# Optimization experiments

Hardware: AMD Instinct MI355X
Metric: run time of the kernel (lower is better)

The kernel has to match this reference:

```python
import jax, jax.numpy as jnp
import numpy as np

N = 20000      # nodes
E = 320000     # edges
IN = 300       # input_channel
HID = 100      # hidden_channel (= heads*out_channels with heads=1)
R = 50         # num_relations
B = 8          # num_bases (the 4th positional arg 'heads'=8 lands on num_bases in PyG RGATConv)
HEADS = 1
CLS = 3
Q = 64         # number of query (aspect) nodes
EPS = 1e-16


def setup_inputs() -> dict:
    key = jax.random.key(0)
    ks = jax.random.split(key, 16)
    x = jax.random.normal(ks[0], (N, IN), jnp.float32)
    edge_index = jax.random.randint(ks[1], (2, E), 0, N)
    edge_type = jax.random.randint(ks[2], (E,), 0, R)
    query_indices = jax.random.randint(ks[3], (Q,), 0, N)

    def w(k, shape, scale):
        return jax.random.normal(k, shape, jnp.float32) * scale

    comp1 = w(ks[4], (R, B), 0.3)
    basis1 = w(ks[5], (B, IN, HEADS * HID), 1.0 / np.sqrt(IN))
    q1 = w(ks[6], (HEADS * HID, HEADS), 0.1)
    k1 = w(ks[7], (HEADS * HID, HEADS), 0.1)
    b1 = jnp.zeros((HEADS * HID,), jnp.float32)
    comp2 = w(ks[8], (R, B), 0.3)
    basis2 = w(ks[9], (B, HID, HEADS * HID), 1.0 / np.sqrt(HID))
    q2 = w(ks[10], (HEADS * HID, HEADS), 0.1)
    k2 = w(ks[11], (HEADS * HID, HEADS), 0.1)
    b2 = jnp.zeros((HEADS * HID,), jnp.float32)
    Wl = w(ks[12], (CLS, HID), 1.0 / np.sqrt(HID))
    bl = jnp.zeros((CLS,), jnp.float32)
    return dict(x=x, edge_index=edge_index, edge_type=edge_type,
                query_indices=query_indices,
                comp1=comp1, basis1=basis1, q1=q1, k1=k1, b1=b1,
                comp2=comp2, basis2=basis2, q2=q2, k2=k2, b2=b2,
                Wl=Wl, bl=bl)


def segment_softmax(alpha, seg, num_segments):
    # numerically-stable softmax over edges grouped by destination node
    m = jax.ops.segment_max(alpha, seg, num_segments=num_segments)  # [N, H]
    e = jnp.exp(alpha - m[seg])
    s = jax.ops.segment_sum(e, seg, num_segments=num_segments)
    return e / (s[seg] + EPS)


def rgat_conv(x, edge_index, edge_type, comp, basis, q, k, b):
    # basis-decomposed per-relation weight: [R, in, H*out]
    W = jnp.einsum('rb,bio->rio', comp, basis)
    # transform every node under every relation once, then gather per edge
    xt = jnp.einsum('ni,rio->nro', x, W)          # [N, R, H*out]
    src, dst = edge_index[0], edge_index[1]        # j -> i (source_to_target)
    xi = xt[dst, edge_type]                        # [E, H*out]
    xj = xt[src, edge_type]                        # [E, H*out]
    qi = xi @ q                                    # [E, H]
    kj = xj @ k                                    # [E, H]
    alpha = jax.nn.leaky_relu(qi + kj, 0.2)        # additive self-attention
    alpha = segment_softmax(alpha, dst, N)         # across-relation softmax
    msg = xj.reshape(E, HEADS, HID) * alpha[:, :, None]
    out = jax.ops.segment_sum(msg, dst, num_segments=N)  # [N, H, out]
    return out.reshape(N, HEADS * HID) + b         # concat=True


def reference(x, edge_index, edge_type, query_indices,
              comp1, basis1, q1, k1, b1,
              comp2, basis2, q2, k2, b2, Wl, bl):
    h = jax.nn.relu(rgat_conv(x, edge_index, edge_type, comp1, basis1, q1, k1, b1))
    h = jax.nn.relu(rgat_conv(h, edge_index, edge_type, comp2, basis2, q2, k2, b2))
    pooled = h[query_indices].mean(axis=0)          # [HID]
    return pooled @ Wl.T + bl                       # [CLS]
```

## Files before the change

### kernel.cpp

```cpp
#include <hip/hip_runtime.h>
#include <math.h>

#define N_NODES 20000
#define E_EDGES 320000
#define IN_CH   300
#define HID     100
#define R_REL   50
#define NB      8
#define CLS     3
#define NQ      64
#define OUTW    800
#define ZW      128
#define SCAN_BLKS ((N_NODES + 255) / 256)

typedef unsigned short ushort_t;
typedef __attribute__((ext_vector_type(8))) short     short8;
typedef __attribute__((ext_vector_type(8))) unsigned short ushort8;
typedef __attribute__((ext_vector_type(4))) float     f32x4;
typedef __attribute__((ext_vector_type(2))) float     f32x2;

__device__ __forceinline__ ushort_t f2bf_rne(float f) {
    unsigned u = __float_as_uint(f);
    unsigned r = (u + 0x7fffu + ((u >> 16) & 1u)) >> 16;
    return (ushort_t)r;
}
__device__ __forceinline__ float bf2f(ushort_t u) {
    return __uint_as_float((unsigned)u << 16);
}

__global__ __launch_bounds__(256) void zero_deg2(int* __restrict__ dd,
                                                 int* __restrict__ ds) {
    int i = blockIdx.x * 256 + threadIdx.x;
    if (i < N_NODES) { dd[i] = 0; ds[i] = 0; }
}

__global__ __launch_bounds__(256) void hist2_kernel(
        const int* __restrict__ ei, int* __restrict__ dd,
        int* __restrict__ ds) {
    int e = blockIdx.x * 256 + threadIdx.x;
    if (e < E_EDGES) {
        atomicAdd(&dd[ei[E_EDGES + e]], 1);
        atomicAdd(&ds[ei[e]], 1);
    }
}

__global__ __launch_bounds__(256) void scan1_kernel(
        const int* __restrict__ deg, int* __restrict__ rowptr,
        int* __restrict__ bsum) {
    __shared__ int s[256];
    int tid = threadIdx.x;
    int idx = blockIdx.x * 256 + tid;
    int v = (idx < N_NODES) ? deg[idx] : 0;
    s[tid] = v; __syncthreads();
    #pragma unroll
    for (int off = 1; off < 256; off <<= 1) {
        int t = (tid >= off) ? s[tid - off] : 0;
        __syncthreads();
        s[tid] += t;
        __syncthreads();
    }
    if (idx < N_NODES) rowptr[idx] = s[tid] - v;
    if (tid == 255) bsum[blockIdx.x] = s[255];
}

__global__ __launch_bounds__(128) void scan2_kernel(int* __restrict__ bsum,
                                                    int* __restrict__ rowptr) {
    __shared__ int s[128];
    int tid = threadIdx.x;
    int v = (tid < SCAN_BLKS) ? bsum[tid] : 0;
    s[tid] = v; __syncthreads();
    #pragma unroll
    for (int off = 1; off < 128; off <<= 1) {
        int t = (tid >= off) ? s[tid - off] : 0;
        __syncthreads();
        s[tid] += t;
        __syncthreads();
    }
    if (tid < SCAN_BLKS) bsum[tid] = s[tid] - v;
    if (tid == 0) rowptr[N_NODES] = E_EDGES;
}

__global__ __launch_bounds__(256) void scan3_kernel(
        int* __restrict__ rowptr, const int* __restrict__ bsum,
        int* __restrict__ cursor) {
    int idx = blockIdx.x * 256 + threadIdx.x;
    if (idx < N_NODES) {
        int v = rowptr[idx] + bsum[blockIdx.x];
        rowptr[idx] = v;
        cursor[idx] = v;
    }
}

__global__ __launch_bounds__(256) void scatter_both(
        const int* __restrict__ ei, const int* __restrict__ et,
        int* __restrict__ cur_d, int* __restrict__ cur_s,
        int* __restrict__ skey, int* __restrict__ skey_s) {
    int e = blockIdx.x * 256 + threadIdx.x;
    if (e >= E_EDGES) return;
    int s = ei[e], d = ei[E_EDGES + e], rt = et[e];
    int p = atomicAdd(&cur_d[d], 1);
    skey[p] = (s << 6) | rt;
    int qp = atomicAdd(&cur_s[s], 1);
    skey_s[qp] = (p << 6) | rt;
}

__global__ __launch_bounds__(256) void split_bt_kernel(
        const float* __restrict__ basis, ushort_t* __restrict__ Bt,
        int K, int Kp) {
    int idx = blockIdx.x * 256 + threadIdx.x;
    if (idx >= OUTW * Kp) return;
    int n = idx / Kp, k = idx - n * Kp;
    int b = n / HID, o = n - b * HID;
    float v = 0.f;
    if (k < K) v = basis[((size_t)b * K + k) * HID + o];
    Bt[idx] = f2bf_rne(v);
}

#define BM 128
#define BN 160
__global__ __launch_bounds__(256) void gemm_mfma(
        const float* __restrict__ A, const ushort_t* __restrict__ Bt,
        float* __restrict__ C, int M, int K, int Kp, int do_relu) {
    __shared__ ushort_t As[BM][32];
    __shared__ ushort_t Bs[BN][32];
    int tid  = threadIdx.x;
    int lane = tid & 63, wave = tid >> 6;
    int ml = lane & 15, quad = lane >> 4;
    int wr = (wave >> 1) * 64, wc = (wave & 1) * 80;
    int row0 = blockIdx.y * BM, col0 = blockIdx.x * BN;
    int ra = tid >> 1, half = tid & 1;
    int gr_a = row0 + ra;
    int sw_a = ra & 3;
    f32x4 acc[4][5] = {};
    int ksteps = Kp >> 5;
    for (int ks = 0; ks < ksteps; ks++) {
        int k0 = ks << 5;
        __syncthreads();
        {
            float vals[16];
            int kb1 = k0 + half * 8;
            int kb2 = kb1 + 16;
            if (gr_a < M) {
                const float* ar = A + (size_t)gr_a * K;
                if (kb1 + 8 <= K) {
                    float4 f0 = *(const float4*)&ar[kb1];
                    float4 f1 = *(const float4*)&ar[kb1 + 4];
                    vals[0]=f0.x; vals[1]=f0.y; vals[2]=f0.z; vals[3]=f0.w;
                    vals[4]=f1.x; vals[5]=f1.y; vals[6]=f1.z; vals[7]=f1.w;
                } else {
                    #pragma unroll
                    for (int i = 0; i < 8; i++)
                        vals[i] = (kb1 + i < K) ? ar[kb1 + i] : 0.f;
                }
                if (kb2 + 8 <= K) {
                    float4 f0 = *(const float4*)&ar[kb2];
                    float4 f1 = *(const float4*)&ar[kb2 + 4];
                    vals[8]=f0.x; vals[9]=f0.y; vals[10]=f0.z; vals[11]=f0.w;
                    vals[12]=f1.x; vals[13]=f1.y; vals[14]=f1.z; vals[15]=f1.w;
                } else {
                    #pragma unroll
                    for (int i = 0; i < 8; i++)
                        vals[8 + i] = (kb2 + i < K) ? ar[kb2 + i] : 0.f;
                }
                if (do_relu)
                    #pragma unroll
                    for (int i = 0; i < 16; i++) vals[i] = fmaxf(vals[i], 0.f);
            } else {
                #pragma unroll
                for (int i = 0; i < 16; i++) vals[i] = 0.f;
            }
            ushort8 h1v, h2v;
            #pragma unroll
            for (int i = 0; i < 8; i++) {
                h1v[i] = f2bf_rne(vals[i]);
                h2v[i] = f2bf_rne(vals[8 + i]);
            }
            int p1 = half ^ sw_a, p2 = (half + 2) ^ sw_a;
            *(ushort8*)&As[ra][p1 * 8] = h1v;
            *(ushort8*)&As[ra][p2 * 8] = h2v;
        }
        for (int t = tid; t < 640; t += 256) {
            int rb = t >> 2, ch = t & 3;
            int ph = ch ^ (rb & 3);
            ushort8 vh = *(const ushort8*)&Bt[(size_t)(col0 + rb) * Kp + k0 + ch * 8];
            *(ushort8*)&Bs[rb][ph * 8] = vh;
        }
        __syncthreads();
        int pq = quad ^ (ml & 3);
        short8 af[4], bf[5];
        #pragma unroll
        for (int mt = 0; mt < 4; mt++)
            af[mt] = *(const short8*)&As[wr + mt * 16 + ml][pq * 8];
        #pragma unroll
        for (int nt = 0; nt < 5; nt++)
            bf[nt] = *(const short8*)&Bs[wc + nt * 16 + ml][pq * 8];
        #pragma unroll
        for (int mt = 0; mt < 4; mt++)
            #pragma unroll
            for (int nt = 0; nt < 5; nt++)
                acc[mt][nt] = __builtin_amdgcn_mfma_f32_16x16x32_bf16(af[mt], bf[nt], acc[mt][nt], 0, 0, 0);
    }
    #pragma unroll
    for (int mt = 0; mt < 4; mt++) {
        #pragma unroll
        for (int nt = 0; nt < 5; nt++) {
            #pragma unroll
            for (int r = 0; r < 4; r++) {
                int grow = row0 + wr + mt * 16 + quad * 4 + r;
                if (grow < M)
                    C[(size_t)grow * OUTW + col0 + wc + nt * 16 + ml] = acc[mt][nt][r];
            }
        }
    }
}

__global__ __launch_bounds__(256) void qbkb_kernel(
        const float* __restrict__ basis, const float* __restrict__ q,
        const float* __restrict__ k, float* __restrict__ qb,
        float* __restrict__ kb, int K) {
    int idx = blockIdx.x * 256 + threadIdx.x;
    if (idx >= K * NB) return;
    int kk = idx >> 3, b = idx & 7;
    const float* br = basis + ((size_t)b * K + kk) * HID;
    float aq = 0.f, ak = 0.f;
    for (int o = 0; o < HID; o++) {
        float v = br[o];
        aq = fmaf(v, q[o], aq);
        ak = fmaf(v, k[o], ak);
    }
    qb[idx] = aq; kb[idx] = ak;
}

__global__ __launch_bounds__(256) void qk2_kernel(
        const float* __restrict__ x, const float* __restrict__ qb,
        const float* __restrict__ kb, float* __restrict__ xbq,
        float* __restrict__ xbk, int K, int do_relu) {
    __shared__ float sqb[320 * NB], skb[320 * NB];
    int tid = threadIdx.x;
    for (int i = tid; i < K * NB; i += 256) { sqb[i] = qb[i]; skb[i] = kb[i]; }
    __syncthreads();
    int idx = blockIdx.x * 256 + tid;
    if (idx >= N_NODES * NB) return;
    int n = idx >> 3, b = idx & 7;
    const float* xr = x + (size_t)n * K;
    float aq = 0.f, ak = 0.f;
    for (int kk = 0; kk < K; kk++) {
        float v = xr[kk];
        if (do_relu) v = fmaxf(v, 0.f);
        aq = fmaf(v, sqb[kk * NB + b], aq);
        ak = fmaf(v, skb[kk * NB + b], ak);
    }
    xbq[idx] = aq;
    xbk[idx] = ak;
}

__global__ __launch_bounds__(256) void compute_z(
        const int* __restrict__ rowptr_s, const int* __restrict__ skey_s,
        const float* __restrict__ comp, const float* __restrict__ xb,
        ushort_t* __restrict__ Z) {
    int wave = threadIdx.x >> 6, lane = threadIdx.x & 63;
    int s = blockIdx.x * 4 + wave;
    if (s >= N_NODES) return;
    int beg = rowptr_s[s], end = rowptr_s[s + 1];
    if (beg == end) return;
    int o = lane * 2;
    f32x2 xrow[NB];
    if (lane < 50) {
        #pragma unroll
        for (int b = 0; b < NB; b++)
            xrow[b] = *(const f32x2*)&xb[(size_t)s * OUTW + b * HID + o];
    }
    for (int p = beg; p < end; p++) {
        int key = skey_s[p];
        int zpos = key >> 6, rt = key & 63;
        const float* cr = comp + rt * NB;
        if (lane < 50) {
            f32x2 z = {0.f, 0.f};
            #pragma unroll
            for (int b = 0; b < NB; b++) z += cr[b] * xrow[b];
            ushort2 zz;
            zz.x = f2bf_rne(z.x);
            zz.y = f2bf_rne(z.y);
            *(ushort2*)&Z[(size_t)zpos * ZW + o] = zz;
        }
    }
}

__global__ __launch_bounds__(256) void msg_soft(
        const int* __restrict__ rowptr, const int* __restrict__ skey,
        const float* __restrict__ comp, const ushort_t* __restrict__ Z,
        const float* __restrict__ xbq, const float* __restrict__ xbk,
        const float* __restrict__ bias, float* __restrict__ h) {
    int wave = threadIdx.x >> 6, lane = threadIdx.x & 63;
    int d = blockIdx.x * 4 + wave;
    if (d >= N_NODES) return;
    int beg = rowptr[d], end = rowptr[d + 1];

    float4 qd0 = *(const float4*)&xbq[d * NB];
    float4 qd1 = *(const float4*)&xbq[d * NB + 4];

    f32x2 acc = {0.f, 0.f};
    float m = -1e30f, l = 0.f;
    int o = lane * 2;

    for (int c0 = beg; c0 < end; c0 += 64) {
        int p = c0 + lane;
        bool valid = p < end;
        float a = -1e30f;
        if (valid) {
            int key = skey[p];
            int s = key >> 6, rt = key & 63;
            const float4 c0v = *(const float4*)&comp[rt * NB];
            const float4 c1v = *(const float4*)&comp[rt * NB + 4];
            const float4 k0v = *(const float4*)&xbk[s * NB];
            const float4 k1v = *(const float4*)&xbk[s * NB + 4];
            float qi = c0v.x*qd0.x + c0v.y*qd0.y + c0v.z*qd0.z + c0v.w*qd0.w
                     + c1v.x*qd1.x + c1v.y*qd1.y + c1v.z*qd1.z + c1v.w*qd1.w;
            float kj = c0v.x*k0v.x + c0v.y*k0v.y + c0v.z*k0v.z + c0v.w*k0v.w
                     + c1v.x*k1v.x + c1v.y*k1v.y + c1v.z*k1v.z + c1v.w*k1v.w;
            a = qi + kj;
            a = a > 0.f ? a : 0.2f * a;
        }
        float cm = a;
        #pragma unroll
        for (int off = 32; off; off >>= 1) cm = fmaxf(cm, __shfl_xor(cm, off));
        float M = fmaxf(m, cm);
        float scale = __expf(m - M);
        acc *= scale; l *= scale; m = M;
        float wgt = valid ? __expf(a - M) : 0.f;
        float cs = wgt;
        #pragma unroll
        for (int off = 32; off; off >>= 1) cs += __shfl_xor(cs, off);
        l += cs;
        int cnt = end - c0; if (cnt > 64) cnt = 64;
        for (int j = 0; j < cnt; j++) {
            float wj = __shfl(wgt, j);
            if (lane < 50) {
                ushort2 zz = *(const ushort2*)&Z[(size_t)(c0 + j) * ZW + o];
                f32x2 zv = {bf2f(zz.x), bf2f(zz.y)};
                acc += wj * zv;
            }
        }
    }
    if (lane < 50) {
        float inv = 1.f / (l + 1e-16f);
        f32x2 r;
        r.x = bias[o]     + acc.x * inv;
        r.y = bias[o + 1] + acc.y * inv;
        *(f32x2*)&h[(size_t)d * HID + o] = r;
    }
}

__global__ __launch_bounds__(128) void head_kernel(
        const float* __restrict__ h2, const int* __restrict__ qidx,
        const float* __restrict__ Wl, const float* __restrict__ bl,
        float* __restrict__ out) {
    __shared__ float pooled[HID];
    int tid = threadIdx.x;
    if (tid < HID) {
        float s = 0.f;
        for (int i = 0; i < NQ; i++)
            s += fmaxf(h2[(size_t)qidx[i] * HID + tid], 0.f);
        pooled[tid] = s * (1.0f / NQ);
    }
    __syncthreads();
    if (tid < CLS) {
        float s = bl[tid];
        for (int o = 0; o < HID; o++) s = fmaf(pooled[o], Wl[tid * HID + o], s);
        out[tid] = s;
    }
}

extern "C" void kernel_launch(void* const* d_in, const int* in_sizes, int n_in,
                              void* d_out, int out_size, void* d_ws, size_t ws_size,
                              hipStream_t stream) {
    const float* x      = (const float*)d_in[0];
    const int*   ei     = (const int*)  d_in[1];
    const int*   et     = (const int*)  d_in[2];
    const int*   qidx   = (const int*)  d_in[3];
    const float* comp1  = (const float*)d_in[4];
    const float* basis1 = (const float*)d_in[5];
    const float* q1     = (const float*)d_in[6];
    const float* k1     = (const float*)d_in[7];
    const float* b1     = (const float*)d_in[8];
    const float* comp2  = (const float*)d_in[9];
    const float* basis2 = (const float*)d_in[10];
    const float* q2     = (const float*)d_in[11];
    const float* k2     = (const float*)d_in[12];
    const float* b2     = (const float*)d_in[13];
    const float* Wl     = (const float*)d_in[14];
    const float* bl     = (const float*)d_in[15];
    float* out = (float*)d_out;

    const int KP1 = 320, KP2 = 128;

    char* w = (char*)d_ws;
    size_t off = 0;
    auto alloc = [&](size_t nbytes) {
        void* p = (void*)(w + off);
        off += ((nbytes + 255) / 256) * 256;
        return p;
    };
    float*    xb     = (float*)alloc((size_t)N_NODES * OUTW * 4);
    ushort_t* Z      = (ushort_t*)alloc((size_t)E_EDGES * ZW * 2);
    float*    h1     = (float*)alloc((size_t)N_NODES * HID * 4);
    float*    h2     = (float*)alloc((size_t)N_NODES * HID * 4);
    ushort_t* Bt     = (ushort_t*)alloc((size_t)OUTW * KP1 * 2);
    float*    xbq    = (float*)alloc((size_t)N_NODES * NB * 4);
    float*    xbk    = (float*)alloc((size_t)N_NODES * NB * 4);
    float*    qb     = (float*)alloc((size_t)KP1 * NB * 4);
    float*    kb     = (float*)alloc((size_t)KP1 * NB * 4);
    int*      deg_d  = (int*)alloc(N_NODES * 4);
    int*      deg_s  = (int*)alloc(N_NODES * 4);
    int*      rp_d   = (int*)alloc((N_NODES + 1) * 4);
    int*      rp_s   = (int*)alloc((N_NODES + 1) * 4);
    int*      cur_d  = (int*)alloc(N_NODES * 4);
    int*      cur_s  = (int*)alloc(N_NODES * 4);
    int*      bsum   = (int*)alloc(SCAN_BLKS * 4);
    int*      skey   = (int*)alloc(E_EDGES * 4);
    int*      skey_s = (int*)alloc(E_EDGES * 4);

    zero_deg2<<<SCAN_BLKS, 256, 0, stream>>>(deg_d, deg_s);
    hist2_kernel<<<(E_EDGES + 255) / 256, 256, 0, stream>>>(ei, deg_d, deg_s);
    scan1_kernel<<<SCAN_BLKS, 256, 0, stream>>>(deg_d, rp_d, bsum);
    scan2_kernel<<<1, 128, 0, stream>>>(bsum, rp_d);
    scan3_kernel<<<SCAN_BLKS, 256, 0, stream>>>(rp_d, bsum, cur_d);
    scan1_kernel<<<SCAN_BLKS, 256, 0, stream>>>(deg_s, rp_s, bsum);
    scan2_kernel<<<1, 128, 0, stream>>>(bsum, rp_s);
    scan3_kernel<<<SCAN_BLKS, 256, 0, stream>>>(rp_s, bsum, cur_s);
    scatter_both<<<(E_EDGES + 255) / 256, 256, 0, stream>>>(ei, et, cur_d, cur_s, skey, skey_s);

    auto layer = [&](const float* input, int K, int Kp, int relu_in,
                     const float* comp, const float* basis, const float* q,
                     const float* k, const float* bias, float* hout) {
        int nb = OUTW * Kp;
        split_bt_kernel<<<(nb + 255) / 256, 256, 0, stream>>>(basis, Bt, K, Kp);
        dim3 g(OUTW / BN, (N_NODES + BM - 1) / BM);
        gemm_mfma<<<g, 256, 0, stream>>>(input, Bt, xb, N_NODES, K, Kp, relu_in);
        qbkb_kernel<<<(K * NB + 255) / 256, 256, 0, stream>>>(basis, q, k, qb, kb, K);
        qk2_kernel<<<(N_NODES * NB + 255) / 256, 256, 0, stream>>>(input, qb, kb, xbq, xbk, K, relu_in);
        compute_z<<<(N_NODES + 3) / 4, 256, 0, stream>>>(rp_s, skey_s, comp, xb, Z);
        msg_soft<<<(N_NODES + 3) / 4, 256, 0, stream>>>(rp_d, skey, comp, Z, xbq, xbk, bias, hout);
    };

    layer(x,  IN_CH, KP1, 0, comp1, basis1, q1, k1, b1, h1);
    layer(h1, HID,   KP2, 1, comp2, basis2, q2, k2, b2, h2);
    head_kernel<<<1, 128, 0, stream>>>(h2, qidx, Wl, bl, out);
}
```

Measured before the change: 439.5 us.

## Store basis-projected features in bf16, shrink GEMM tile, restage qk2 via LDS

The GEMM output xb is now written as bf16 instead of fp32, halving the write traffic and compute_z's read traffic. The GEMM row tile drops from 128 to 64, so there are more blocks and fewer accumulators per wave. Z row width shrinks from 128 to 100 elements, cutting the padded per-edge storage. qk2 now stages 32 input rows in shared memory and reads qb/kb from global memory instead of shared. The bf16 intermediate adds rounding error to the features.

```diff
diff --git a/kernel.cpp b/kernel.cpp
--- a/kernel.cpp
+++ b/kernel.cpp
@@ -10,7 +10,7 @@
 #define CLS     3
 #define NQ      64
 #define OUTW    800
-#define ZW      128
+#define ZW      100
 #define SCAN_BLKS ((N_NODES + 255) / 256)
 
 typedef unsigned short ushort_t;
@@ -116,68 +116,52 @@
     Bt[idx] = f2bf_rne(v);
 }
 
-#define BM 128
+#define BM 64
 #define BN 160
 __global__ __launch_bounds__(256) void gemm_mfma(
         const float* __restrict__ A, const ushort_t* __restrict__ Bt,
-        float* __restrict__ C, int M, int K, int Kp, int do_relu) {
+        ushort_t* __restrict__ xbh, int M, int K, int Kp, int do_relu) {
     __shared__ ushort_t As[BM][32];
     __shared__ ushort_t Bs[BN][32];
     int tid  = threadIdx.x;
     int lane = tid & 63, wave = tid >> 6;
     int ml = lane & 15, quad = lane >> 4;
-    int wr = (wave >> 1) * 64, wc = (wave & 1) * 80;
+    int wr = (wave >> 1) * 32, wc = (wave & 1) * 80;
     int row0 = blockIdx.y * BM, col0 = blockIdx.x * BN;
-    int ra = tid >> 1, half = tid & 1;
+    int ra = tid >> 2, ch_a = tid & 3;
     int gr_a = row0 + ra;
-    int sw_a = ra & 3;
-    f32x4 acc[4][5] = {};
+    f32x4 acc[2][5] = {};
     int ksteps = Kp >> 5;
     for (int ks = 0; ks < ksteps; ks++) {
         int k0 = ks << 5;
         __syncthreads();
         {
-            float vals[16];
-            int kb1 = k0 + half * 8;
-            int kb2 = kb1 + 16;
+            float vals[8];
+            int kb = k0 + ch_a * 8;
             if (gr_a < M) {
                 const float* ar = A + (size_t)gr_a * K;
-                if (kb1 + 8 <= K) {
-                    float4 f0 = *(const float4*)&ar[kb1];
-                    float4 f1 = *(const float4*)&ar[kb1 + 4];
+                if (kb + 8 <= K) {
+                    float4 f0 = *(const float4*)&ar[kb];
+                    float4 f1 = *(const float4*)&ar[kb + 4];
                     vals[0]=f0.x; vals[1]=f0.y; vals[2]=f0.z; vals[3]=f0.w;
                     vals[4]=f1.x; vals[5]=f1.y; vals[6]=f1.z; vals[7]=f1.w;
                 } else {
                     #pragma unroll
                     for (int i = 0; i < 8; i++)
-                        vals[i] = (kb1 + i < K) ? ar[kb1 + i] : 0.f;
-                }
-                if (kb2 + 8 <= K) {
-                    float4 f0 = *(const float4*)&ar[kb2];
-                    float4 f1 = *(const float4*)&ar[kb2 + 4];
-                    vals[8]=f0.x; vals[9]=f0.y; vals[10]=f0.z; vals[11]=f0.w;
-                    vals[12]=f1.x; vals[13]=f1.y; vals[14]=f1.z; vals[15]=f1.w;
-                } else {
-                    #pragma unroll
-                    for (int i = 0; i < 8; i++)
-                        vals[8 + i] = (kb2 + i < K) ? ar[kb2 + i] : 0.f;
+                        vals[i] = (kb + i < K) ? ar[kb + i] : 0.f;
                 }
                 if (do_relu)
                     #pragma unroll
-                    for (int i = 0; i < 16; i++) vals[i] = fmaxf(vals[i], 0.f);
+                    for (int i = 0; i < 8; i++) vals[i] = fmaxf(vals[i], 0.f);
             } else {
                 #pragma unroll
-                for (int i = 0; i < 16; i++) vals[i] = 0.f;
+                for (int i = 0; i < 8; i++) vals[i] = 0.f;
             }
-            ushort8 h1v, h2v;
+            ushort8 hv;
             #pragma unroll
-            for (int i = 0; i < 8; i++) {
-                h1v[i] = f2bf_rne(vals[i]);
-                h2v[i] = f2bf_rne(vals[8 + i]);
-            }
-            int p1 = half ^ sw_a, p2 = (half + 2) ^ sw_a;
-            *(ushort8*)&As[ra][p1 * 8] = h1v;
-            *(ushort8*)&As[ra][p2 * 8] = h2v;
+            for (int i = 0; i < 8; i++) hv[i] = f2bf_rne(vals[i]);
+            int p1 = ch_a ^ (ra & 3);
+            *(ushort8*)&As[ra][p1 * 8] = hv;
         }
         for (int t = tid; t < 640; t += 256) {
             int rb = t >> 2, ch = t & 3;
@@ -187,28 +171,29 @@
         }
         __syncthreads();
         int pq = quad ^ (ml & 3);
-        short8 af[4], bf[5];
-        #pragma unroll
-        for (int mt = 0; mt < 4; mt++)
+        short8 af[2], bf[5];
+        #pragma unroll
+        for (int mt = 0; mt < 2; mt++)
             af[mt] = *(const short8*)&As[wr + mt * 16 + ml][pq * 8];
         #pragma unroll
         for (int nt = 0; nt < 5; nt++)
             bf[nt] = *(const short8*)&Bs[wc + nt * 16 + ml][pq * 8];
         #pragma unroll
-        for (int mt = 0; mt < 4; mt++)
+        for (int mt = 0; mt < 2; mt++)
             #pragma unroll
             for (int nt = 0; nt < 5; nt++)
                 acc[mt][nt] = __builtin_amdgcn_mfma_f32_16x16x32_bf16(af[mt], bf[nt], acc[mt][nt], 0, 0, 0);
     }
     #pragma unroll
-    for (int mt = 0; mt < 4; mt++) {
+    for (int mt = 0; mt < 2; mt++) {
         #pragma unroll
         for (int nt = 0; nt < 5; nt++) {
             #pragma unroll
             for (int r = 0; r < 4; r++) {
                 int grow = row0 + wr + mt * 16 + quad * 4 + r;
                 if (grow < M)
-                    C[(size_t)grow * OUTW + col0 + wc + nt * 16 + ml] = acc[mt][nt][r];
+                    xbh[(size_t)grow * OUTW + col0 + wc + nt * 16 + ml] =
+                        f2bf_rne(acc[mt][nt][r]);
             }
         }
     }
@@ -231,32 +216,41 @@
     qb[idx] = aq; kb[idx] = ak;
 }
 
+#define QKN 32
 __global__ __launch_bounds__(256) void qk2_kernel(
         const float* __restrict__ x, const float* __restrict__ qb,
         const float* __restrict__ kb, float* __restrict__ xbq,
         float* __restrict__ xbk, int K, int do_relu) {
-    __shared__ float sqb[320 * NB], skb[320 * NB];
+    __shared__ float sx[QKN][301];
     int tid = threadIdx.x;
-    for (int i = tid; i < K * NB; i += 256) { sqb[i] = qb[i]; skb[i] = kb[i]; }
+    int n0 = blockIdx.x * QKN;
+    for (int r = 0; r < QKN; r++) {
+        int gn = n0 + r;
+        if (gn >= N_NODES) break;
+        const float* xr = x + (size_t)gn * K;
+        for (int c = tid; c < K; c += 256) {
+            float v = xr[c];
+            if (do_relu) v = fmaxf(v, 0.f);
+            sx[r][c] = v;
+        }
+    }
     __syncthreads();
-    int idx = blockIdx.x * 256 + tid;
-    if (idx >= N_NODES * NB) return;
-    int n = idx >> 3, b = idx & 7;
-    const float* xr = x + (size_t)n * K;
+    int n = tid >> 3, b = tid & 7;
+    int gn = n0 + n;
+    if (gn >= N_NODES) return;
     float aq = 0.f, ak = 0.f;
     for (int kk = 0; kk < K; kk++) {
-        float v = xr[kk];
-        if (do_relu) v = fmaxf(v, 0.f);
-        aq = fmaf(v, sqb[kk * NB + b], aq);
-        ak = fmaf(v, skb[kk * NB + b], ak);
-    }
-    xbq[idx] = aq;
-    xbk[idx] = ak;
+        float v = sx[n][kk];
+        aq = fmaf(v, qb[kk * NB + b], aq);
+        ak = fmaf(v, kb[kk * NB + b], ak);
+    }
+    xbq[gn * NB + b] = aq;
+    xbk[gn * NB + b] = ak;
 }
 
 __global__ __launch_bounds__(256) void compute_z(
         const int* __restrict__ rowptr_s, const int* __restrict__ skey_s,
-        const float* __restrict__ comp, const float* __restrict__ xb,
+        const float* __restrict__ comp, const ushort_t* __restrict__ xbh,
         ushort_t* __restrict__ Z) {
     int wave = threadIdx.x >> 6, lane = threadIdx.x & 63;
     int s = blockIdx.x * 4 + wave;
@@ -267,8 +261,11 @@
     f32x2 xrow[NB];
     if (lane < 50) {
         #pragma unroll
-        for (int b = 0; b < NB; b++)
-            xrow[b] = *(const f32x2*)&xb[(size_t)s * OUTW + b * HID + o];
+        for (int b = 0; b < NB; b++) {
+            ushort2 xx = *(const ushort2*)&xbh[(size_t)s * OUTW + b * HID + o];
+            xrow[b].x = bf2f(xx.x);
+            xrow[b].y = bf2f(xx.y);
+        }
     }
     for (int p = beg; p < end; p++) {
         int key = skey_s[p];
@@ -401,7 +398,7 @@
         off += ((nbytes + 255) / 256) * 256;
         return p;
     };
-    float*    xb     = (float*)alloc((size_t)N_NODES * OUTW * 4);
+    ushort_t* xbh    = (ushort_t*)alloc((size_t)N_NODES * OUTW * 2);
     ushort_t* Z      = (ushort_t*)alloc((size_t)E_EDGES * ZW * 2);
     float*    h1     = (float*)alloc((size_t)N_NODES * HID * 4);
     float*    h2     = (float*)alloc((size_t)N_NODES * HID * 4);
@@ -436,10 +433,10 @@
         int nb = OUTW * Kp;
         split_bt_kernel<<<(nb + 255) / 256, 256, 0, stream>>>(basis, Bt, K, Kp);
         dim3 g(OUTW / BN, (N_NODES + BM - 1) / BM);
-        gemm_mfma<<<g, 256, 0, stream>>>(input, Bt, xb, N_NODES, K, Kp, relu_in);
+        gemm_mfma<<<g, 256, 0, stream>>>(input, Bt, xbh, N_NODES, K, Kp, relu_in);
         qbkb_kernel<<<(K * NB + 255) / 256, 256, 0, stream>>>(basis, q, k, qb, kb, K);
-        qk2_kernel<<<(N_NODES * NB + 255) / 256, 256, 0, stream>>>(input, qb, kb, xbq, xbk, K, relu_in);
-        compute_z<<<(N_NODES + 3) / 4, 256, 0, stream>>>(rp_s, skey_s, comp, xb, Z);
+        qk2_kernel<<<(N_NODES + QKN - 1) / QKN, 256, 0, stream>>>(input, qb, kb, xbq, xbk, K, relu_in);
+        compute_z<<<(N_NODES + 3) / 4, 256, 0, stream>>>(rp_s, skey_s, comp, xbh, Z);
         msg_soft<<<(N_NODES + 3) / 4, 256, 0, stream>>>(rp_d, skey, comp, Z, xbq, xbk, bias, hout);
     };
 
```

Result: slower. 456.3 us (+3.8%).
